# Kernel tuning notes

Hardware: AMD Instinct MI355X
Metric: run time of the kernel (lower is better)

## Reference

```python
import jax, jax.numpy as jnp
import numpy as np

IN_DIM, OUT_DIM, NUM, K = 256, 128, 16, 3
BATCH = 2048
MONO = ((0, 1), (1, -1))  # (input dim index, direction)


def _make_grid():
    # linspace over grid_range, then extend k knots on each side with uniform step h
    lo, hi = -1.0, 1.0
    h = (hi - lo) / NUM
    pts = np.linspace(lo, hi, NUM + 1)
    ext = np.concatenate([lo + h * np.arange(-K, 0), pts, hi + h * np.arange(1, K + 1)])
    return jnp.asarray(np.tile(ext, (IN_DIM, 1)), dtype=jnp.float32)  # (in_dim, num+2k+1)


def _b_batch(x, grid, k):
    # de-Boor B-spline basis. x: (B, in), grid: (in, G). Returns (B, in, G-k-1).
    xg = x[:, :, None]
    g = grid[None, :, :]
    B = ((xg >= g[:, :, :-1]) & (xg < g[:, :, 1:])).astype(x.dtype)
    for p in range(1, k + 1):
        left = (xg - g[:, :, :-(p + 1)]) / (g[:, :, p:-1] - g[:, :, :-(p + 1)]) * B[:, :, :-1]
        right = (g[:, :, p + 1:] - xg) / (g[:, :, p + 1:] - g[:, :, 1:-p]) * B[:, :, 1:]
        B = left + right
    return B


def setup_inputs() -> dict:
    key = jax.random.key(0)
    k1, k2, k3, k4 = jax.random.split(key, 4)
    inv_sqrt_in = 1.0 / np.sqrt(IN_DIM)
    x = 0.4 * jax.random.normal(k1, (BATCH, IN_DIM), dtype=jnp.float32)
    coef = 0.1 * jax.random.normal(k2, (IN_DIM, OUT_DIM, NUM + K), dtype=jnp.float32)
    scale_sp_raw = jnp.ones((IN_DIM, OUT_DIM), dtype=jnp.float32) * inv_sqrt_in
    scale_base = (jax.random.uniform(k3, (IN_DIM, OUT_DIM), dtype=jnp.float32) * 2.0 - 1.0) * inv_sqrt_in
    grid = _make_grid()
    mask = jnp.ones((IN_DIM, OUT_DIM), dtype=jnp.float32)
    base_mask = jnp.ones((IN_DIM, OUT_DIM), dtype=jnp.float32)
    for dim, _ in MONO:
        base_mask = base_mask.at[dim, :].set(0.0)
    return {"x": x, "coef": coef, "scale_sp_raw": scale_sp_raw, "scale_base": scale_base,
            "grid": grid, "mask": mask, "base_mask": base_mask}


def reference(x, coef, scale_sp_raw, scale_base, grid, mask, base_mask):
    bs = x.shape[0]
    preacts = jnp.broadcast_to(x[:, None, :], (bs, OUT_DIM, IN_DIM))
    # monotonic reparameterization: softplus + cumsum over spline-coefficient axis
    for dim, direction in MONO:
        delta = jnp.cumsum(jax.nn.softplus(coef[dim]), axis=-1)  # (out, num+k)
        coef = coef.at[dim].set(direction * delta)
    # coef2curve: basis (B, in, num+k) contracted with coef (in, out, num+k)
    basis = _b_batch(x, grid, K)
    y = jnp.einsum('bid,iod->bio', basis, coef)  # (B, in, out)
    postspline = jnp.transpose(y, (0, 2, 1))
    scale_sp = jax.nn.softplus(scale_sp_raw)
    y = scale_sp[None, :, :] * y
    base = base_mask * scale_base[None, :, :] * jax.nn.silu(x)[:, :, None]
    y = y + base
    y = mask[None, :, :] * y
    postacts = jnp.transpose(y, (0, 2, 1))
    out = jnp.sum(y, axis=1)  # (B, out)
    return out, preacts, postacts, postspline
```

## Files before the change

### kernel.cpp

```cpp
#include <hip/hip_runtime.h>
#include <math.h>

#define IN_DIM   256
#define OUT_DIM  128
#define NCOEF    19
#define BATCH    2048
#define BT       4
#define TILE_F   (IN_DIM * NCOEF)
#define MAIN_BLOCKS (BATCH / BT)
#define FILL_BLOCKS (BATCH / 2)

typedef float f32x4 __attribute__((ext_vector_type(4)));

__device__ __forceinline__ float softplus_f(float v) {
  return (v > 20.0f) ? v : log1pf(expf(v));
}

__device__ __forceinline__ void load_lds16(const float* g, float* l) {
  __builtin_amdgcn_global_load_lds(
      (const __attribute__((address_space(1))) void*)g,
      (__attribute__((address_space(3))) void*)l,
      16, 0, 0);
}

__device__ __forceinline__ void stage_tile(const float* src, float* dst, int tid) {
  load_lds16(src + tid * 4,        dst + tid * 4);
  load_lds16(src + 2048 + tid * 4, dst + 2048 + tid * 4);
  if (tid < 192) load_lds16(src + 4096 + tid * 4, dst + 4096 + tid * 4);
}

__global__ void kan_prep(const float* __restrict__ coef,
                         const float* __restrict__ ssp,
                         const float* __restrict__ sbase,
                         const float* __restrict__ mask,
                         const float* __restrict__ bmask,
                         float* __restrict__ coefT,
                         float* __restrict__ At,
                         float* __restrict__ Bt) {
  int g = blockIdx.x * 256 + threadIdx.x;
  int o = g >> 8;
  int i = g & 255;
  const float* src = coef + ((size_t)i * OUT_DIM + o) * NCOEF;
  float c[NCOEF];
#pragma unroll
  for (int d = 0; d < NCOEF; ++d) c[d] = src[d];
  if (i < 2) {
    float dir = (i == 0) ? 1.0f : -1.0f;
    float acc = 0.0f;
#pragma unroll
    for (int d = 0; d < NCOEF; ++d) { acc += softplus_f(c[d]); c[d] = dir * acc; }
  }
  float* dst = coefT + (size_t)o * TILE_F + i;
#pragma unroll
  for (int d = 0; d < NCOEF; ++d) dst[d * IN_DIM] = c[d];
  int io = i * OUT_DIM + o;
  float m = mask[io];
  At[g] = m * softplus_f(ssp[io]);
  Bt[g] = m * bmask[io] * sbase[io];
}

__device__ __forceinline__ float wave_reduce(float v) {
  int t;
  t = __builtin_amdgcn_update_dpp(0, __float_as_int(v), 0x111, 0xf, 0xf, true); v += __int_as_float(t);
  t = __builtin_amdgcn_update_dpp(0, __float_as_int(v), 0x112, 0xf, 0xf, true); v += __int_as_float(t);
  t = __builtin_amdgcn_update_dpp(0, __float_as_int(v), 0x114, 0xf, 0xf, true); v += __int_as_float(t);
  t = __builtin_amdgcn_update_dpp(0, __float_as_int(v), 0x118, 0xf, 0xf, true); v += __int_as_float(t);
  t = __builtin_amdgcn_update_dpp(0, __float_as_int(v), 0x142, 0xa, 0xf, true); v += __int_as_float(t);
  t = __builtin_amdgcn_update_dpp(0, __float_as_int(v), 0x143, 0xc, 0xf, true); v += __int_as_float(t);
  return v;
}

__global__ __launch_bounds__(512, 6) void kan_main(
    const float* __restrict__ x,
    const float* __restrict__ coefT,
    const float* __restrict__ At,
    const float* __restrict__ Bt,
    float* __restrict__ out,
    float* __restrict__ preacts,
    float* __restrict__ postacts,
    float* __restrict__ postspline) {
  __shared__ __align__(16) float s_coef[2][TILE_F];
  __shared__ float s_out[BT][OUT_DIM][4];

  const int tid = threadIdx.x;
  const int bid = blockIdx.x;

  if (bid >= MAIN_BLOCKS) {
    const int g    = bid - MAIN_BLOCKS;
    const int w    = tid >> 6;
    const int lane = tid & 63;
    const int b    = 2 * g + (w >> 2);
    const int o0   = (w & 3) * 32;
    const f32x4 xr = *(const f32x4*)(x + (size_t)b * IN_DIM + lane * 4);
    float* dst = preacts + (((size_t)b * OUT_DIM + o0) * IN_DIM) + lane * 4;
#pragma unroll 8
    for (int k = 0; k < 32; ++k)
      __builtin_nontemporal_store(xr, (f32x4*)(dst + (size_t)k * IN_DIM));
    return;
  }

  const int i    = tid & 255;
  const int bsub = tid >> 8;
  const int wq   = (tid >> 6) & 3;
  const int b0   = bid * BT;

  float xv[2], sl[2], wv[2][4];
  int   wl[2][4];

#pragma unroll
  for (int bb = 0; bb < 2; ++bb) {
    int b = b0 + bsub * 2 + bb;
    float xx = x[(size_t)b * IN_DIM + i];
    xv[bb] = xx;
    sl[bb] = xx / (1.0f + expf(-xx));

    float tpos = (xx + 1.375f) * 8.0f;
    int j = (int)floorf(tpos);
    bool valid = (j >= 0) && (j <= 21);
    int jc = valid ? j : 3;

    float N[4] = {1.0f, 0.0f, 0.0f, 0.0f};
#pragma unroll
    for (int p = 1; p <= 3; ++p) {
      const float inv = (p == 1) ? 8.0f : ((p == 2) ? 4.0f : (8.0f / 3.0f));
      float Np[4] = {0.0f, 0.0f, 0.0f, 0.0f};
#pragma unroll
      for (int m = 0; m < 4; ++m) {
        if (m <= p) {
          float ga = -1.375f + 0.125f * (float)(jc + m - p);
          float v = 0.0f;
          if (m > 0) v += (xx - ga) * inv * N[m - 1];
          if (m < p) v += ((ga + 0.125f * (float)(p + 1)) - xx) * inv * N[m];
          Np[m] = v;
        }
      }
#pragma unroll
      for (int m = 0; m < 4; ++m) N[m] = Np[m];
    }
#pragma unroll
    for (int r = 0; r < 4; ++r) {
      int dr = jc - 3 + r;
      bool ok = valid && (dr >= 0) && (dr <= 18);
      wv[bb][r] = ok ? N[r] : 0.0f;
      wl[bb][r] = (ok ? dr : 0) * IN_DIM + i;
    }
  }

  stage_tile(coefT, &s_coef[0][0], tid);
  float a_cur = At[i];
  float b_cur = Bt[i];
  __syncthreads();

  size_t off0 = ((size_t)(b0 + bsub * 2)     * OUT_DIM) * IN_DIM + i;
  size_t off1 = ((size_t)(b0 + bsub * 2 + 1) * OUT_DIM) * IN_DIM + i;

#pragma unroll 2
  for (int o = 0; o < OUT_DIM; ++o) {
    const int cur = o & 1;
    const float* sc = &s_coef[cur][0];

    if (o + 1 < OUT_DIM)
      stage_tile(coefT + (size_t)(o + 1) * TILE_F, &s_coef[cur ^ 1][0], tid);
    asm volatile("" ::: "memory");

    float a_nxt = 0.0f, b_nxt = 0.0f;
    if (o + 1 < OUT_DIM) {
      a_nxt = At[(o + 1) * IN_DIM + i];
      b_nxt = Bt[(o + 1) * IN_DIM + i];
    }

#pragma unroll
    for (int bb = 0; bb < 2; ++bb) {
      int bl = bsub * 2 + bb;
      float sp = wv[bb][0] * sc[wl[bb][0]]
               + wv[bb][1] * sc[wl[bb][1]]
               + wv[bb][2] * sc[wl[bb][2]]
               + wv[bb][3] * sc[wl[bb][3]];
      float ya = a_cur * sp + b_cur * sl[bb];

      size_t off = (bb == 0 ? off0 : off1) + (size_t)o * IN_DIM;
      __builtin_nontemporal_store(sp, postspline + off);
      __builtin_nontemporal_store(ya, postacts   + off);

      float red = wave_reduce(ya);
      if ((tid & 63) == 63) s_out[bl][o][wq] = red;
    }

    asm volatile("s_waitcnt vmcnt(4)" ::: "memory");
    __builtin_amdgcn_s_barrier();

    a_cur = a_nxt;
    b_cur = b_nxt;
  }

  __syncthreads();
  {
    int bl = tid >> 7;
    int o  = tid & 127;
    float s = s_out[bl][o][0] + s_out[bl][o][1] + s_out[bl][o][2] + s_out[bl][o][3];
    out[(size_t)(b0 + bl) * OUT_DIM + o] = s;
  }
}

extern "C" void kernel_launch(void* const* d_in, const int* in_sizes, int n_in,
                              void* d_out, int out_size, void* d_ws, size_t ws_size,
                              hipStream_t stream) {
  (void)in_sizes; (void)n_in; (void)out_size; (void)ws_size;

  const float* x     = (const float*)d_in[0];
  const float* coef  = (const float*)d_in[1];
  const float* ssp   = (const float*)d_in[2];
  const float* sbase = (const float*)d_in[3];
  const float* mask  = (const float*)d_in[5];
  const float* bmask = (const float*)d_in[6];

  float* coefT = (float*)d_ws;
  float* At    = coefT + (size_t)OUT_DIM * IN_DIM * NCOEF;
  float* Bt    = At + (size_t)OUT_DIM * IN_DIM;

  float* out        = (float*)d_out;
  float* preacts    = out + (size_t)BATCH * OUT_DIM;
  float* postacts   = preacts + (size_t)BATCH * OUT_DIM * IN_DIM;
  float* postspline = postacts + (size_t)BATCH * OUT_DIM * IN_DIM;

  kan_prep<<<(OUT_DIM * IN_DIM) / 256, 256, 0, stream>>>(coef, ssp, sbase, mask, bmask,
                                                         coefT, At, Bt);
  kan_main<<<MAIN_BLOCKS + FILL_BLOCKS, 512, 0, stream>>>(x, coefT, At, Bt,
                                                          out, preacts, postacts, postspline);
}
```

Before: 175.8 us.

## Stage two coefficient tiles per barrier and move output reduction to separate kernel

The main loop now handles two output columns per iteration, using four LDS coefficient buffers so it needs half as many barriers, and prefetches two tiles ahead. The per-block LDS buffer for partial row sums is gone. Wave partial sums go to a workspace buffer, and a new small kernel adds the four partials into the final output. LDS use rises from about 47KB to about 78KB per block, which can lower occupancy, and the change adds a third launch plus extra global traffic for the partial sums.

New measurement: 192.8 us. 1.1x slower.

```diff
diff --git a/kernel.cpp b/kernel.cpp
--- a/kernel.cpp
+++ b/kernel.cpp
@@ -75,12 +75,11 @@
     const float* __restrict__ coefT,
     const float* __restrict__ At,
     const float* __restrict__ Bt,
-    float* __restrict__ out,
+    float* __restrict__ out_part,
     float* __restrict__ preacts,
     float* __restrict__ postacts,
     float* __restrict__ postspline) {
-  __shared__ __align__(16) float s_coef[2][TILE_F];
-  __shared__ float s_out[BT][OUT_DIM][4];
+  __shared__ __align__(16) float s_coef[4][TILE_F];
 
   const int tid = threadIdx.x;
   const int bid = blockIdx.x;
@@ -146,60 +145,62 @@
     }
   }
 
-  stage_tile(coefT, &s_coef[0][0], tid);
-  float a_cur = At[i];
-  float b_cur = Bt[i];
+  stage_tile(coefT,          &s_coef[0][0], tid);
+  stage_tile(coefT + TILE_F, &s_coef[1][0], tid);
+  float a0 = At[i],          b0s = Bt[i];
+  float a1 = At[IN_DIM + i], b1s = Bt[IN_DIM + i];
   __syncthreads();
 
   size_t off0 = ((size_t)(b0 + bsub * 2)     * OUT_DIM) * IN_DIM + i;
   size_t off1 = ((size_t)(b0 + bsub * 2 + 1) * OUT_DIM) * IN_DIM + i;
 
-#pragma unroll 2
-  for (int o = 0; o < OUT_DIM; ++o) {
-    const int cur = o & 1;
-    const float* sc = &s_coef[cur][0];
-
-    if (o + 1 < OUT_DIM)
-      stage_tile(coefT + (size_t)(o + 1) * TILE_F, &s_coef[cur ^ 1][0], tid);
+#define KAN_ONE_O(o_, SC_, A_, B_)                                        \
+  do {                                                                    \
+    const float* sc_ = (SC_);                                             \
+    _Pragma("unroll")                                                     \
+    for (int bb = 0; bb < 2; ++bb) {                                      \
+      float sp = wv[bb][0] * sc_[wl[bb][0]] + wv[bb][1] * sc_[wl[bb][1]]  \
+               + wv[bb][2] * sc_[wl[bb][2]] + wv[bb][3] * sc_[wl[bb][3]]; \
+      float ya = (A_) * sp + (B_) * sl[bb];                               \
+      size_t off = (bb == 0 ? off0 : off1) + (size_t)(o_) * IN_DIM;       \
+      __builtin_nontemporal_store(sp, postspline + off);                  \
+      __builtin_nontemporal_store(ya, postacts   + off);                  \
+      float red = wave_reduce(ya);                                        \
+      if ((tid & 63) == 63) {                                             \
+        int bl_ = bsub * 2 + bb;                                          \
+        __builtin_nontemporal_store(                                      \
+            red, out_part + (((size_t)(b0 + bl_) * OUT_DIM + (o_)) << 2) + wq); \
+      }                                                                   \
+    }                                                                     \
+  } while (0)
+
+  for (int r = 0; r < OUT_DIM; r += 2) {
+    const int p = (r >> 1) & 1;
+    const int on2 = (r + 2 < OUT_DIM) ? r + 2 : OUT_DIM - 1;
+    const int on3 = (r + 3 < OUT_DIM) ? r + 3 : OUT_DIM - 1;
+    stage_tile(coefT + (size_t)on2 * TILE_F, &s_coef[2 * (p ^ 1)][0],     tid);
+    stage_tile(coefT + (size_t)on3 * TILE_F, &s_coef[2 * (p ^ 1) + 1][0], tid);
     asm volatile("" ::: "memory");
 
-    float a_nxt = 0.0f, b_nxt = 0.0f;
-    if (o + 1 < OUT_DIM) {
-      a_nxt = At[(o + 1) * IN_DIM + i];
-      b_nxt = Bt[(o + 1) * IN_DIM + i];
-    }
-
-#pragma unroll
-    for (int bb = 0; bb < 2; ++bb) {
-      int bl = bsub * 2 + bb;
-      float sp = wv[bb][0] * sc[wl[bb][0]]
-               + wv[bb][1] * sc[wl[bb][1]]
-               + wv[bb][2] * sc[wl[bb][2]]
-               + wv[bb][3] * sc[wl[bb][3]];
-      float ya = a_cur * sp + b_cur * sl[bb];
-
-      size_t off = (bb == 0 ? off0 : off1) + (size_t)o * IN_DIM;
-      __builtin_nontemporal_store(sp, postspline + off);
-      __builtin_nontemporal_store(ya, postacts   + off);
-
-      float red = wave_reduce(ya);
-      if ((tid & 63) == 63) s_out[bl][o][wq] = red;
-    }
-
-    asm volatile("s_waitcnt vmcnt(4)" ::: "memory");
+    float a2 = At[on2 * IN_DIM + i], b2 = Bt[on2 * IN_DIM + i];
+    float a3 = At[on3 * IN_DIM + i], b3 = Bt[on3 * IN_DIM + i];
+
+    KAN_ONE_O(r,     &s_coef[2 * p][0],     a0, b0s);
+    KAN_ONE_O(r + 1, &s_coef[2 * p + 1][0], a1, b1s);
+
+    asm volatile("s_waitcnt vmcnt(12)" ::: "memory");
     __builtin_amdgcn_s_barrier();
 
-    a_cur = a_nxt;
-    b_cur = b_nxt;
-  }
-
-  __syncthreads();
-  {
-    int bl = tid >> 7;
-    int o  = tid & 127;
-    float s = s_out[bl][o][0] + s_out[bl][o][1] + s_out[bl][o][2] + s_out[bl][o][3];
-    out[(size_t)(b0 + bl) * OUT_DIM + o] = s;
-  }
+    a0 = a2; b0s = b2; a1 = a3; b1s = b3;
+  }
+#undef KAN_ONE_O
+}
+
+__global__ __launch_bounds__(512) void kan_out(const float* __restrict__ out_part,
+                                               float* __restrict__ out) {
+  int g = blockIdx.x * 512 + threadIdx.x;
+  const float* p = out_part + ((size_t)g << 2);
+  out[g] = (p[0] + p[1]) + (p[2] + p[3]);
 }
 
 extern "C" void kernel_launch(void* const* d_in, const int* in_sizes, int n_in,
@@ -214,9 +215,10 @@
   const float* mask  = (const float*)d_in[5];
   const float* bmask = (const float*)d_in[6];
 
-  float* coefT = (float*)d_ws;
-  float* At    = coefT + (size_t)OUT_DIM * IN_DIM * NCOEF;
-  float* Bt    = At + (size_t)OUT_DIM * IN_DIM;
+  float* coefT    = (float*)d_ws;
+  float* At       = coefT + (size_t)OUT_DIM * IN_DIM * NCOEF;
+  float* Bt       = At + (size_t)OUT_DIM * IN_DIM;
+  float* out_part = Bt + (size_t)OUT_DIM * IN_DIM;
 
   float* out        = (float*)d_out;
   float* preacts    = out + (size_t)BATCH * OUT_DIM;
@@ -226,5 +228,7 @@
   kan_prep<<<(OUT_DIM * IN_DIM) / 256, 256, 0, stream>>>(coef, ssp, sbase, mask, bmask,
                                                          coefT, At, Bt);
   kan_main<<<MAIN_BLOCKS + FILL_BLOCKS, 512, 0, stream>>>(x, coefT, At, Bt,
-                                                          out, preacts, postacts, postspline);
-}
+                                                          out_part, preacts, postacts,
+                                                          postspline);
+  kan_out<<<(BATCH * OUT_DIM) / 512, 512, 0, stream>>>(out_part, out);
+}
```
